# Kernel optimization log

Measured on AMD Instinct MI355X. Metric: run time of the kernel, lower is better.

The kernel has to match this reference:

```python
import jax, jax.numpy as jnp
import numpy as np
import math

N_NODES = 100000
N_EDGES = 1600000
IN_DIM = 32
OUT_DIM = 32

def setup_inputs() -> dict:
    key = jax.random.key(0)
    k1, k2, k3, k4 = jax.random.split(key, 4)
    X = jax.random.normal(k1, (N_NODES, IN_DIM), dtype=jnp.float32)
    src_idx = jax.random.randint(k2, (N_EDGES,), 0, N_NODES, dtype=jnp.int64)
    dst_idx = jax.random.randint(k3, (N_EDGES,), 0, N_NODES, dtype=jnp.int64)
    # weights init: uniform(-stdv, stdv), stdv = 1/sqrt(output_dim)
    stdv = 1.0 / math.sqrt(OUT_DIM)
    W = jax.random.uniform(k4, (IN_DIM, OUT_DIM), dtype=jnp.float32,
                           minval=-stdv, maxval=stdv)
    return {"X": X, "W": W, "src_idx": src_idx, "dst_idx": dst_idx}

def reference(X, W, src_idx, dst_idx):
    # GIN sum-aggregation SpMM: agg[i] = sum_{j in N(i)} X[j]
    agg = jax.ops.segment_sum(X[src_idx], dst_idx, num_segments=N_NODES)
    # dense GEMM: X_prime = agg @ W
    return agg @ W
```

## Files before the change

### kernel.cpp

```cpp
#include <hip/hip_runtime.h>

#define N_DIM 32
#define NPB 64
#define NB_FINE_MAX 2048
#define NC_MAX 128
#define CSH 10
#define CAPC 18432
#define CAPFINE 1280
#define CEPB 4096
#define CT 512
#define CAPF 2048
#define MAXCH 10
#define CAP 2048

__device__ __forceinline__ unsigned f2bf_rne(float f) {
    unsigned u = __float_as_uint(f);
    return (u + 0x7FFFu + ((u >> 16) & 1u)) >> 16;
}
__device__ __forceinline__ float bf2f(unsigned h) {
    return __uint_as_float(h << 16);
}

__global__ __launch_bounds__(256) void k_gemm(const float* __restrict__ X,
                                              const float* __restrict__ W,
                                              unsigned* __restrict__ Y,
                                              int* __restrict__ cursors,
                                              int n_nodes) {
    __shared__ float Wlds[N_DIM * N_DIM];
    const int t = threadIdx.x;
    if (blockIdx.x == 0)
        for (int i = t; i < NC_MAX + NB_FINE_MAX; i += 256) cursors[i] = 0;
    for (int i = t; i < N_DIM * N_DIM; i += 256) Wlds[i] = W[i];
    __syncthreads();

    const int r = blockIdx.x * 256 + t;
    if (r >= n_nodes) return;

    float x[N_DIM];
    const float4* xr = (const float4*)(X + (size_t)r * N_DIM);
#pragma unroll
    for (int i = 0; i < N_DIM / 4; ++i) {
        float4 v = xr[i];
        x[4 * i + 0] = v.x; x[4 * i + 1] = v.y;
        x[4 * i + 2] = v.z; x[4 * i + 3] = v.w;
    }
    float acc[N_DIM];
#pragma unroll
    for (int c = 0; c < N_DIM; ++c) acc[c] = 0.0f;
#pragma unroll
    for (int k = 0; k < N_DIM; ++k) {
        const float xk = x[k];
#pragma unroll
        for (int c = 0; c < N_DIM; ++c)
            acc[c] = fmaf(xk, Wlds[k * N_DIM + c], acc[c]);
    }
    unsigned yp[16];
#pragma unroll
    for (int q = 0; q < 16; ++q)
        yp[q] = f2bf_rne(acc[2 * q]) | (f2bf_rne(acc[2 * q + 1]) << 16);
    uint4* yr = (uint4*)(Y + (size_t)r * 16);
#pragma unroll
    for (int i = 0; i < 4; ++i)
        yr[i] = make_uint4(yp[4 * i], yp[4 * i + 1], yp[4 * i + 2], yp[4 * i + 3]);
}

__global__ __launch_bounds__(CT) void k_cpart(const int* __restrict__ src,
                                              const int* __restrict__ dst,
                                              int* __restrict__ cursorC0,
                                              int* __restrict__ tmp,
                                              int n_edges, int ncoarse) {
    __shared__ int h[NC_MAX];
    __shared__ int gb[NC_MAX];
    const int t = threadIdx.x;
    if (t < NC_MAX) h[t] = 0;
    __syncthreads();
    const int start = blockIdx.x * CEPB;

    int vw[CEPB / CT], cw[CEPB / CT], rw[CEPB / CT];
#pragma unroll
    for (int k = 0; k < CEPB / CT; ++k) {
        int e = start + t + k * CT;
        if (e < n_edges) {
            int d = dst[e];
            int c = d >> CSH;
            cw[k] = c;
            vw[k] = src[e] | ((d & 1023) << 17);
            rw[k] = atomicAdd(&h[c], 1);
        } else {
            cw[k] = -1;
        }
    }
    __syncthreads();
    if (t < ncoarse) {
        int c = h[t];
        gb[t] = c ? atomicAdd(&cursorC0[t], c) : 0;
    }
    __syncthreads();
#pragma unroll
    for (int k = 0; k < CEPB / CT; ++k)
        if (cw[k] >= 0) {
            int idx = gb[cw[k]] + rw[k];
            if (idx < CAPC) tmp[cw[k] * CAPC + idx] = vw[k];
        }
}

__global__ __launch_bounds__(256) void k_fpart(const int* __restrict__ tmp,
                                               const int* __restrict__ cursorC0,
                                               int* __restrict__ cursorF0,
                                               int* __restrict__ pairs,
                                               int ncoarse) {
    __shared__ int cnt[16], gpos[16];
    const int t = threadIdx.x;
    const int c = blockIdx.x;
    const int lenC = min(cursorC0[c], CAPC);

    for (int chunk = blockIdx.y; chunk * CAPF < lenC; chunk += gridDim.y) {
        const int start = chunk * CAPF;
        const int n = min(CAPF, lenC - start);
        if (t < 16) cnt[t] = 0;
        __syncthreads();
        int pv[CAPF / 256], rv[CAPF / 256];
#pragma unroll
        for (int k = 0; k < CAPF / 256; ++k) {
            int i = t + k * 256;
            if (i < n) {
                int p = tmp[c * CAPC + start + i];
                pv[k] = p;
                rv[k] = atomicAdd(&cnt[(p >> 23) & 15], 1);
            } else {
                pv[k] = -1;
            }
        }
        __syncthreads();
        if (t < 16) gpos[t] = cnt[t] ? atomicAdd(&cursorF0[16 * c + t], cnt[t]) : 0;
        __syncthreads();
#pragma unroll
        for (int k = 0; k < CAPF / 256; ++k) {
            if (pv[k] >= 0) {
                int p = pv[k];
                int f = (p >> 23) & 15;
                int idx = gpos[f] + rv[k];
                if (idx < CAPFINE)
                    pairs[(size_t)(16 * c + f) * CAPFINE + idx] = p & 0x7FFFFF;
            }
        }
        __syncthreads();
    }
}

__device__ __forceinline__ void addv(float* acc, uint4 v) {
    acc[0] += bf2f(v.x & 0xFFFFu); acc[1] += bf2f(v.x >> 16);
    acc[2] += bf2f(v.y & 0xFFFFu); acc[3] += bf2f(v.y >> 16);
    acc[4] += bf2f(v.z & 0xFFFFu); acc[5] += bf2f(v.z >> 16);
    acc[6] += bf2f(v.w & 0xFFFFu); acc[7] += bf2f(v.w >> 16);
}

__global__ __launch_bounds__(256) void k_agg(const uint4* __restrict__ Y4,
                                             const int* __restrict__ cursorF0,
                                             const int* __restrict__ pairs,
                                             float* __restrict__ out,
                                             int n_nodes) {
    __shared__ int sbin[CAP];
    __shared__ int cnt[NPB];
    __shared__ int cst[NPB];
    __shared__ int excl[NPB];

    const int t = threadIdx.x;
    const int b = blockIdx.x;
    const int len = min(cursorF0[b], CAPFINE);
    const size_t segbase = (size_t)b * CAPFINE;
    const int g = t >> 2;
    const int l = t & 3;

    float acc[8];
#pragma unroll
    for (int i = 0; i < 8; ++i) acc[i] = 0.0f;

    for (int cbase = 0; cbase < len; cbase += CAP) {
        const int n = min(CAP, len - cbase);
        if (t < NPB) cnt[t] = 0;
        __syncthreads();
        int pv[CAP / 256], rv[CAP / 256];
#pragma unroll
        for (int k = 0; k < CAP / 256; ++k) {
            int i = t + k * 256;
            if (i < n) {
                int p = pairs[segbase + cbase + i];
                pv[k] = p;
                rv[k] = atomicAdd(&cnt[p >> 17], 1);
            } else {
                pv[k] = -1;
            }
        }
        __syncthreads();
        if (t < 64) {
            int c0 = cnt[t];
            int c = c0;
#pragma unroll
            for (int off = 1; off < 64; off <<= 1) {
                int u = __shfl_up(c, off, 64);
                if (t >= off) c += u;
            }
            cst[t] = c;
            excl[t] = c - c0;
        }
        __syncthreads();
#pragma unroll
        for (int k = 0; k < CAP / 256; ++k) {
            if (pv[k] >= 0) {
                int p = pv[k];
                sbin[excl[p >> 17] + rv[k]] = p & 0x1FFFF;
            }
        }
        __syncthreads();
        const int s1 = cst[g];
        const int s0 = s1 - cnt[g];
        for (int e = s0; e < s1; e += 4) {
            const int m = s1 - e;
            int i0 = sbin[e];
            int i1 = sbin[e + ((m > 1) ? 1 : 0)];
            int i2 = sbin[e + ((m > 2) ? 2 : 0)];
            int i3 = sbin[e + ((m > 3) ? 3 : 0)];
            uint4 v0 = Y4[(size_t)i0 * 4 + l];
            uint4 v1 = Y4[(size_t)i1 * 4 + l];
            uint4 v2 = Y4[(size_t)i2 * 4 + l];
            uint4 v3 = Y4[(size_t)i3 * 4 + l];
            addv(acc, v0);
            if (m > 1) addv(acc, v1);
            if (m > 2) addv(acc, v2);
            if (m > 3) addv(acc, v3);
        }
        __syncthreads();
    }

    const int node = b * NPB + g;
    if (node < n_nodes) {
        ((float4*)out)[(size_t)node * 8 + 2 * l] =
            make_float4(acc[0], acc[1], acc[2], acc[3]);
        ((float4*)out)[(size_t)node * 8 + 2 * l + 1] =
            make_float4(acc[4], acc[5], acc[6], acc[7]);
    }
}

extern "C" void kernel_launch(void* const* d_in, const int* in_sizes, int n_in,
                              void* d_out, int out_size, void* d_ws, size_t ws_size,
                              hipStream_t stream) {
    const float* X   = (const float*)d_in[0];
    const float* W   = (const float*)d_in[1];
    const int*   src = (const int*)d_in[2];
    const int*   dst = (const int*)d_in[3];
    float* out = (float*)d_out;

    const int n_nodes = in_sizes[0] / N_DIM;
    const int n_edges = in_sizes[2];
    const int nb = (n_nodes + NPB - 1) / NPB;
    const int ncoarse = (n_nodes + 1023) / 1024;

    unsigned* Y   = (unsigned*)d_ws;
    int* cursorC0 = (int*)(Y + (size_t)n_nodes * 16);
    int* cursorF0 = cursorC0 + NC_MAX;
    int* tmp      = cursorF0 + NB_FINE_MAX;
    int* pairs    = tmp + (size_t)ncoarse * CAPC;

    const int nblk_g = (n_nodes + 255) / 256;
    const int nblk_c = (n_edges + CEPB - 1) / CEPB;

    k_gemm<<<nblk_g, 256, 0, stream>>>(X, W, Y, cursorC0, n_nodes);
    k_cpart<<<nblk_c, CT, 0, stream>>>(src, dst, cursorC0, tmp, n_edges, ncoarse);
    k_fpart<<<dim3(ncoarse, MAXCH), 256, 0, stream>>>(tmp, cursorC0, cursorF0, pairs, ncoarse);
    k_agg<<<nb, 256, 0, stream>>>((const uint4*)Y, cursorF0, pairs, out, n_nodes);
}
```

Before: 131.4 us.

## Fuse GEMM and coarse edge partition into one heterogeneous launch

Merges the node GEMM and the coarse edge-partition kernels into one launch, splitting work by block index so the two independent stages can run concurrently on the GPU. Cursor zeroing moves to a memset, and the GEMM block now covers 512 rows. The aggregation kernel drops its chunk loop because each fine bin is capped at CAPFINE entries, which removes a loop and some barriers. The memset adds a launch of its own, and the mixed blocks compete for the same resources.

After: 126.3 us. 1.04x faster.

```diff
diff --git a/kernel.cpp b/kernel.cpp
--- a/kernel.cpp
+++ b/kernel.cpp
@@ -8,10 +8,10 @@
 #define CAPC 18432
 #define CAPFINE 1280
 #define CEPB 4096
-#define CT 512
+#define FT 512
+#define GROWS 512
 #define CAPF 2048
 #define MAXCH 10
-#define CAP 2048
 
 __device__ __forceinline__ unsigned f2bf_rne(float f) {
     unsigned u = __float_as_uint(f);
@@ -21,87 +21,85 @@
     return __uint_as_float(h << 16);
 }
 
-__global__ __launch_bounds__(256) void k_gemm(const float* __restrict__ X,
+__global__ __launch_bounds__(FT) void k_fused(const float* __restrict__ X,
                                               const float* __restrict__ W,
                                               unsigned* __restrict__ Y,
-                                              int* __restrict__ cursors,
-                                              int n_nodes) {
-    __shared__ float Wlds[N_DIM * N_DIM];
-    const int t = threadIdx.x;
-    if (blockIdx.x == 0)
-        for (int i = t; i < NC_MAX + NB_FINE_MAX; i += 256) cursors[i] = 0;
-    for (int i = t; i < N_DIM * N_DIM; i += 256) Wlds[i] = W[i];
-    __syncthreads();
-
-    const int r = blockIdx.x * 256 + t;
-    if (r >= n_nodes) return;
-
-    float x[N_DIM];
-    const float4* xr = (const float4*)(X + (size_t)r * N_DIM);
-#pragma unroll
-    for (int i = 0; i < N_DIM / 4; ++i) {
-        float4 v = xr[i];
-        x[4 * i + 0] = v.x; x[4 * i + 1] = v.y;
-        x[4 * i + 2] = v.z; x[4 * i + 3] = v.w;
-    }
-    float acc[N_DIM];
-#pragma unroll
-    for (int c = 0; c < N_DIM; ++c) acc[c] = 0.0f;
-#pragma unroll
-    for (int k = 0; k < N_DIM; ++k) {
-        const float xk = x[k];
-#pragma unroll
-        for (int c = 0; c < N_DIM; ++c)
-            acc[c] = fmaf(xk, Wlds[k * N_DIM + c], acc[c]);
-    }
-    unsigned yp[16];
-#pragma unroll
-    for (int q = 0; q < 16; ++q)
-        yp[q] = f2bf_rne(acc[2 * q]) | (f2bf_rne(acc[2 * q + 1]) << 16);
-    uint4* yr = (uint4*)(Y + (size_t)r * 16);
-#pragma unroll
-    for (int i = 0; i < 4; ++i)
-        yr[i] = make_uint4(yp[4 * i], yp[4 * i + 1], yp[4 * i + 2], yp[4 * i + 3]);
-}
-
-__global__ __launch_bounds__(CT) void k_cpart(const int* __restrict__ src,
+                                              const int* __restrict__ src,
                                               const int* __restrict__ dst,
                                               int* __restrict__ cursorC0,
                                               int* __restrict__ tmp,
-                                              int n_edges, int ncoarse) {
+                                              int n_nodes, int n_edges,
+                                              int ncoarse, int nblk_g) {
+    __shared__ float Wlds[N_DIM * N_DIM];
     __shared__ int h[NC_MAX];
     __shared__ int gb[NC_MAX];
     const int t = threadIdx.x;
-    if (t < NC_MAX) h[t] = 0;
-    __syncthreads();
-    const int start = blockIdx.x * CEPB;
-
-    int vw[CEPB / CT], cw[CEPB / CT], rw[CEPB / CT];
-#pragma unroll
-    for (int k = 0; k < CEPB / CT; ++k) {
-        int e = start + t + k * CT;
-        if (e < n_edges) {
-            int d = dst[e];
-            int c = d >> CSH;
-            cw[k] = c;
-            vw[k] = src[e] | ((d & 1023) << 17);
-            rw[k] = atomicAdd(&h[c], 1);
-        } else {
-            cw[k] = -1;
-        }
-    }
-    __syncthreads();
-    if (t < ncoarse) {
-        int c = h[t];
-        gb[t] = c ? atomicAdd(&cursorC0[t], c) : 0;
-    }
-    __syncthreads();
-#pragma unroll
-    for (int k = 0; k < CEPB / CT; ++k)
-        if (cw[k] >= 0) {
-            int idx = gb[cw[k]] + rw[k];
-            if (idx < CAPC) tmp[cw[k] * CAPC + idx] = vw[k];
-        }
+
+    if (blockIdx.x < nblk_g) {
+        for (int i = t; i < N_DIM * N_DIM; i += FT) Wlds[i] = W[i];
+        __syncthreads();
+        const int r = blockIdx.x * GROWS + t;
+        if (r >= n_nodes) return;
+
+        float x[N_DIM];
+        const float4* xr = (const float4*)(X + (size_t)r * N_DIM);
+#pragma unroll
+        for (int i = 0; i < N_DIM / 4; ++i) {
+            float4 v = xr[i];
+            x[4 * i + 0] = v.x; x[4 * i + 1] = v.y;
+            x[4 * i + 2] = v.z; x[4 * i + 3] = v.w;
+        }
+        float acc[N_DIM];
+#pragma unroll
+        for (int c = 0; c < N_DIM; ++c) acc[c] = 0.0f;
+#pragma unroll
+        for (int k = 0; k < N_DIM; ++k) {
+            const float xk = x[k];
+#pragma unroll
+            for (int c = 0; c < N_DIM; ++c)
+                acc[c] = fmaf(xk, Wlds[k * N_DIM + c], acc[c]);
+        }
+        unsigned yp[16];
+#pragma unroll
+        for (int q = 0; q < 16; ++q)
+            yp[q] = f2bf_rne(acc[2 * q]) | (f2bf_rne(acc[2 * q + 1]) << 16);
+        uint4* yr = (uint4*)(Y + (size_t)r * 16);
+#pragma unroll
+        for (int i = 0; i < 4; ++i)
+            yr[i] = make_uint4(yp[4 * i], yp[4 * i + 1],
+                               yp[4 * i + 2], yp[4 * i + 3]);
+    } else {
+        if (t < NC_MAX) h[t] = 0;
+        __syncthreads();
+        const int start = (blockIdx.x - nblk_g) * CEPB;
+
+        int vw[CEPB / FT], cw[CEPB / FT], rw[CEPB / FT];
+#pragma unroll
+        for (int k = 0; k < CEPB / FT; ++k) {
+            int e = start + t + k * FT;
+            if (e < n_edges) {
+                int d = dst[e];
+                int c = d >> CSH;
+                cw[k] = c;
+                vw[k] = src[e] | ((d & 1023) << 17);
+                rw[k] = atomicAdd(&h[c], 1);
+            } else {
+                cw[k] = -1;
+            }
+        }
+        __syncthreads();
+        if (t < ncoarse) {
+            int c = h[t];
+            gb[t] = c ? atomicAdd(&cursorC0[t], c) : 0;
+        }
+        __syncthreads();
+#pragma unroll
+        for (int k = 0; k < CEPB / FT; ++k)
+            if (cw[k] >= 0) {
+                int idx = gb[cw[k]] + rw[k];
+                if (idx < CAPC) tmp[cw[k] * CAPC + idx] = vw[k];
+            }
+    }
 }
 
 __global__ __launch_bounds__(256) void k_fpart(const int* __restrict__ tmp,
@@ -160,7 +158,7 @@
                                              const int* __restrict__ pairs,
                                              float* __restrict__ out,
                                              int n_nodes) {
-    __shared__ int sbin[CAP];
+    __shared__ int sbin[CAPFINE];
     __shared__ int cnt[NPB];
     __shared__ int cst[NPB];
     __shared__ int excl[NPB];
@@ -172,65 +170,63 @@
     const int g = t >> 2;
     const int l = t & 3;
 
+    if (t < NPB) cnt[t] = 0;
+    __syncthreads();
+
+    int pv[CAPFINE / 256], rv[CAPFINE / 256];
+#pragma unroll
+    for (int k = 0; k < CAPFINE / 256; ++k) {
+        int i = t + k * 256;
+        if (i < len) {
+            int p = pairs[segbase + i];
+            pv[k] = p;
+            rv[k] = atomicAdd(&cnt[p >> 17], 1);
+        } else {
+            pv[k] = -1;
+        }
+    }
+    __syncthreads();
+    if (t < 64) {
+        int c0 = cnt[t];
+        int c = c0;
+#pragma unroll
+        for (int off = 1; off < 64; off <<= 1) {
+            int u = __shfl_up(c, off, 64);
+            if (t >= off) c += u;
+        }
+        cst[t] = c;
+        excl[t] = c - c0;
+    }
+    __syncthreads();
+#pragma unroll
+    for (int k = 0; k < CAPFINE / 256; ++k) {
+        if (pv[k] >= 0) {
+            int p = pv[k];
+            sbin[excl[p >> 17] + rv[k]] = p & 0x1FFFF;
+        }
+    }
+    __syncthreads();
+
     float acc[8];
 #pragma unroll
     for (int i = 0; i < 8; ++i) acc[i] = 0.0f;
 
-    for (int cbase = 0; cbase < len; cbase += CAP) {
-        const int n = min(CAP, len - cbase);
-        if (t < NPB) cnt[t] = 0;
-        __syncthreads();
-        int pv[CAP / 256], rv[CAP / 256];
-#pragma unroll
-        for (int k = 0; k < CAP / 256; ++k) {
-            int i = t + k * 256;
-            if (i < n) {
-                int p = pairs[segbase + cbase + i];
-                pv[k] = p;
-                rv[k] = atomicAdd(&cnt[p >> 17], 1);
-            } else {
-                pv[k] = -1;
-            }
-        }
-        __syncthreads();
-        if (t < 64) {
-            int c0 = cnt[t];
-            int c = c0;
-#pragma unroll
-            for (int off = 1; off < 64; off <<= 1) {
-                int u = __shfl_up(c, off, 64);
-                if (t >= off) c += u;
-            }
-            cst[t] = c;
-            excl[t] = c - c0;
-        }
-        __syncthreads();
-#pragma unroll
-        for (int k = 0; k < CAP / 256; ++k) {
-            if (pv[k] >= 0) {
-                int p = pv[k];
-                sbin[excl[p >> 17] + rv[k]] = p & 0x1FFFF;
-            }
-        }
-        __syncthreads();
-        const int s1 = cst[g];
-        const int s0 = s1 - cnt[g];
-        for (int e = s0; e < s1; e += 4) {
-            const int m = s1 - e;
-            int i0 = sbin[e];
-            int i1 = sbin[e + ((m > 1) ? 1 : 0)];
-            int i2 = sbin[e + ((m > 2) ? 2 : 0)];
-            int i3 = sbin[e + ((m > 3) ? 3 : 0)];
-            uint4 v0 = Y4[(size_t)i0 * 4 + l];
-            uint4 v1 = Y4[(size_t)i1 * 4 + l];
-            uint4 v2 = Y4[(size_t)i2 * 4 + l];
-            uint4 v3 = Y4[(size_t)i3 * 4 + l];
-            addv(acc, v0);
-            if (m > 1) addv(acc, v1);
-            if (m > 2) addv(acc, v2);
-            if (m > 3) addv(acc, v3);
-        }
-        __syncthreads();
+    const int s1 = cst[g];
+    const int s0 = s1 - cnt[g];
+    for (int e = s0; e < s1; e += 4) {
+        const int m = s1 - e;
+        int i0 = sbin[e];
+        int i1 = sbin[e + ((m > 1) ? 1 : 0)];
+        int i2 = sbin[e + ((m > 2) ? 2 : 0)];
+        int i3 = sbin[e + ((m > 3) ? 3 : 0)];
+        uint4 v0 = Y4[(size_t)i0 * 4 + l];
+        uint4 v1 = Y4[(size_t)i1 * 4 + l];
+        uint4 v2 = Y4[(size_t)i2 * 4 + l];
+        uint4 v3 = Y4[(size_t)i3 * 4 + l];
+        addv(acc, v0);
+        if (m > 1) addv(acc, v1);
+        if (m > 2) addv(acc, v2);
+        if (m > 3) addv(acc, v3);
     }
 
     const int node = b * NPB + g;
@@ -262,11 +258,14 @@
     int* tmp      = cursorF0 + NB_FINE_MAX;
     int* pairs    = tmp + (size_t)ncoarse * CAPC;
 
-    const int nblk_g = (n_nodes + 255) / 256;
+    const int nblk_g = (n_nodes + GROWS - 1) / GROWS;
     const int nblk_c = (n_edges + CEPB - 1) / CEPB;
 
-    k_gemm<<<nblk_g, 256, 0, stream>>>(X, W, Y, cursorC0, n_nodes);
-    k_cpart<<<nblk_c, CT, 0, stream>>>(src, dst, cursorC0, tmp, n_edges, ncoarse);
-    k_fpart<<<dim3(ncoarse, MAXCH), 256, 0, stream>>>(tmp, cursorC0, cursorF0, pairs, ncoarse);
+    hipMemsetAsync(cursorC0, 0, (size_t)(NC_MAX + NB_FINE_MAX) * sizeof(int), stream);
+
+    k_fused<<<nblk_g + nblk_c, FT, 0, stream>>>(X, W, Y, src, dst, cursorC0, tmp,
+                                                n_nodes, n_edges, ncoarse, nblk_g);
+    k_fpart<<<dim3(ncoarse, MAXCH), 256, 0, stream>>>(tmp, cursorC0, cursorF0,
+                                                      pairs, ncoarse);
     k_agg<<<nb, 256, 0, stream>>>((const uint4*)Y, cursorF0, pairs, out, n_nodes);
 }
```
